# Kernel tuning notes

Measured on AMD Instinct MI355X. Metric: run time of the kernel, lower is better.

The kernel has to match this reference:

```python
import jax, jax.numpy as jnp
import numpy as np

B, T, P, H, D = 16, 32, 14, 12, 64
L = P * P           # 196 patch tokens (cls token stripped by [:, :, 1:])
DM = H * D          # 768 = d_model
S = 16              # n_synos


def _conv2d(x, w, b):
    # stride 1, padding ksize//2 with odd ksize == SAME
    y = jax.lax.conv_general_dilated(x, w, (1, 1), 'SAME',
                                     dimension_numbers=('NCHW', 'OIHW', 'NCHW'))
    return y + b[None, :, None, None]


def _layernorm(x, g, b, eps=1e-5):
    mu = x.mean(-1, keepdims=True)
    var = ((x - mu) ** 2).mean(-1, keepdims=True)
    return (x - mu) * jax.lax.rsqrt(var + eps) * g + b


def setup_inputs():
    key = jax.random.key(0)
    ks = jax.random.split(key, 8)
    return {
        'q': jax.random.normal(ks[0], (B, T, L + 1, H, D), jnp.float32),
        'k': jax.random.normal(ks[1], (B, T, L + 1, H, D), jnp.float32),
        'v': jax.random.normal(ks[2], (B, T, L + 1, H, D), jnp.float32),
        # t_conv: Conv2d(2*n_head -> 1, ksize_t=3), init normal(std=1e-3), zero bias
        't_conv_w': jax.random.normal(ks[3], (1, 2 * H, 3, 3), jnp.float32) * 1e-3,
        't_conv_b': jnp.zeros((1,), jnp.float32),
        # t_proj: LayerNorm(T^2), Linear(T^2->T), GELU, Linear(T->T^2)
        'ln_g': jnp.ones((T * T,), jnp.float32),
        'ln_b': jnp.zeros((T * T,), jnp.float32),
        'w1': jax.random.normal(ks[4], (T * T, T), jnp.float32) * 0.03,
        'b1': jnp.zeros((T,), jnp.float32),
        'w2': jax.random.normal(ks[5], (T, T * T), jnp.float32) * 0.1,
        'b2': jnp.zeros((T * T,), jnp.float32),
        # p_conv: Conv2d(T^2 -> 1, ksize_s=3)
        'p_conv_w': jax.random.normal(ks[6], (1, T * T, 3, 3), jnp.float32) * 1e-3,
        'p_conv_b': jnp.zeros((1,), jnp.float32),
        # syno_embedding (zeros in torch init; randn here for a non-degenerate test)
        'syno': jax.random.normal(ks[7], (S, DM), jnp.float32) * 0.02,
    }


def reference(q, k, v, t_conv_w, t_conv_b, ln_g, ln_b, w1, b1, w2, b2,
              p_conv_w, p_conv_b, syno):
    scale = 1.0 / jnp.sqrt(jnp.float32(D))
    # ---------------- temporal detection ----------------
    affs = []
    for a in (q, k):  # t_attrs = ['q', 'k']
        x = jnp.transpose(a[:, :, 1:], (0, 2, 1, 3, 4))      # (B, L, T, H, D)
        aff = jnp.einsum('nlqhc,nlkhc->nlqkh', x * scale, x)  # (B, L, T, T, H)
        aff = jax.nn.softmax(aff, axis=-2)                    # softmax over k
        affs.append(jnp.transpose(aff.reshape(B * L, T, T, H), (0, 3, 1, 2)))
    aff = jnp.concatenate(affs, axis=1)                       # (B*L, 2H, T, T)
    aff = _conv2d(aff, t_conv_w, t_conv_b)                    # (B*L, 1, T, T)
    aff = aff.reshape(B, P, P, T * T)                         # (B, P, P, T^2)
    h = _layernorm(aff, ln_g, ln_b)
    h = jax.nn.gelu(h @ w1 + b1, approximate=False) @ w2 + b2
    aff = aff + h
    aff = jnp.transpose(aff, (0, 3, 1, 2))                    # (B, T^2, P, P)
    y_t = _conv2d(aff, p_conv_w, p_conv_b).reshape(B, P * P)  # (B, 196)
    # ---------------- spatial detection -----------------
    kk = k[:, :, 1:].reshape(B, T, L, DM)
    vv = v[:, :, 1:].reshape(B, T, L, DM)
    s_aff = jax.nn.softmax(
        jnp.einsum('qw,ntkw->ntqk', syno / jnp.sqrt(jnp.float32(DM)), kk),
        axis=-1)                                              # (B, T, S, L)
    s_mix = jnp.einsum('ntql,ntlw->ntqw', s_aff, vv)          # (B, T, S, DM)
    y_s = s_mix.reshape(B, T * S, DM).mean(axis=1)            # (B, 768)
    return (y_t, y_s)
```

## Files before the change

kernel.cpp:

```cpp
#include <hip/hip_runtime.h>
#include <math.h>

#define T_ 32
#define P_ 14
#define H_ 12
#define D_ 64
#define L_ 196
#define DM_ 768
#define S_ 16

__global__ __launch_bounds__(256)
void temporal_kernel(const float* __restrict__ q, const float* __restrict__ k,
                     const float* __restrict__ tw, const float* __restrict__ tbias,
                     const float* __restrict__ lng, const float* __restrict__ lnb,
                     const float* __restrict__ w1, const float* __restrict__ b1,
                     const float* __restrict__ w2, const float* __restrict__ b2,
                     float* __restrict__ affbuf)
{
    const int l = blockIdx.x;
    const int b = blockIdx.y;
    const int tid = threadIdx.x;

    __shared__ float Xs[T_ * 64];
    __shared__ float As[T_ * 37];
    __shared__ float nls[1024];
    __shared__ float scratch[256];
    __shared__ float h1s[32];
    __shared__ float redv[8];

    const int pi = tid >> 3;
    const int pj = (tid & 7) << 2;
    float cacc0 = 0.f, cacc1 = 0.f, cacc2 = 0.f, cacc3 = 0.f;

    const int gi = (tid >> 4) << 1;
    const int gj = tid & 15;

    const int t_load = tid >> 3;
    const int d8 = tid & 7;

    for (int ch = 0; ch < 24; ++ch) {
        const float* src = (ch < H_) ? q : k;
        const int h = (ch < H_) ? ch : ch - H_;
        {
            const float* rowp = src + (((size_t)(b * T_ + t_load) * 197 + 1 + l) * DM_) + h * D_;
            float4 v0 = *(const float4*)(rowp + (d8 << 2));
            float4 v1 = *(const float4*)(rowp + (d8 << 2) + 32);
            const int sw = t_load & 15;
            *(float4*)&Xs[(t_load << 6) + (((d8    ) ^ sw) << 2)] = v0;
            *(float4*)&Xs[(t_load << 6) + (((d8 + 8) ^ sw) << 2)] = v1;
        }
        __syncthreads();
        {
            float g00 = 0.f, g01 = 0.f, g10 = 0.f, g11 = 0.f;
            const int swa0 = gi & 15, swa1 = (gi + 1) & 15;
            const int swb = gj;
            #pragma unroll
            for (int c4 = 0; c4 < 16; ++c4) {
                float4 a0  = *(const float4*)&Xs[( gi     << 6) + ((c4 ^ swa0) << 2)];
                float4 a1  = *(const float4*)&Xs[((gi + 1) << 6) + ((c4 ^ swa1) << 2)];
                float4 b0  = *(const float4*)&Xs[( gj     << 6) + ((c4 ^ swb) << 2)];
                float4 b1v = *(const float4*)&Xs[((gj + 16) << 6) + ((c4 ^ swb) << 2)];
                g00 += a0.x * b0.x  + a0.y * b0.y  + a0.z * b0.z  + a0.w * b0.w;
                g01 += a0.x * b1v.x + a0.y * b1v.y + a0.z * b1v.z + a0.w * b1v.w;
                g10 += a1.x * b0.x  + a1.y * b0.y  + a1.z * b0.z  + a1.w * b0.w;
                g11 += a1.x * b1v.x + a1.y * b1v.y + a1.z * b1v.z + a1.w * b1v.w;
            }
            const float scale = 0.125f;
            As[ gi      * 37 + gj     ] = g00 * scale;
            As[ gi      * 37 + gj + 16] = g01 * scale;
            As[(gi + 1) * 37 + gj     ] = g10 * scale;
            As[(gi + 1) * 37 + gj + 16] = g11 * scale;
        }
        __syncthreads();
        {
            float v0 = As[pi * 37 + pj    ];
            float v1 = As[pi * 37 + pj + 1];
            float v2 = As[pi * 37 + pj + 2];
            float v3 = As[pi * 37 + pj + 3];
            float m = fmaxf(fmaxf(v0, v1), fmaxf(v2, v3));
            m = fmaxf(m, __shfl_xor(m, 1, 8));
            m = fmaxf(m, __shfl_xor(m, 2, 8));
            m = fmaxf(m, __shfl_xor(m, 4, 8));
            v0 = __expf(v0 - m); v1 = __expf(v1 - m);
            v2 = __expf(v2 - m); v3 = __expf(v3 - m);
            float s = v0 + v1 + v2 + v3;
            s += __shfl_xor(s, 1, 8);
            s += __shfl_xor(s, 2, 8);
            s += __shfl_xor(s, 4, 8);
            float r = 1.f / s;
            As[pi * 37 + pj    ] = v0 * r;
            As[pi * 37 + pj + 1] = v1 * r;
            As[pi * 37 + pj + 2] = v2 * r;
            As[pi * 37 + pj + 3] = v3 * r;
        }
        __syncthreads();
        {
            float wc[9];
            #pragma unroll
            for (int u = 0; u < 9; ++u) wc[u] = tw[ch * 9 + u];
            #pragma unroll
            for (int di = 0; di < 3; ++di) {
                int r = pi + di - 1;
                if ((unsigned)r < (unsigned)T_) {
                    float c0 = (pj - 1 >= 0) ? As[r * 37 + pj - 1] : 0.f;
                    float c1 = As[r * 37 + pj    ];
                    float c2 = As[r * 37 + pj + 1];
                    float c3 = As[r * 37 + pj + 2];
                    float c4v = As[r * 37 + pj + 3];
                    float c5 = (pj + 4 < T_) ? As[r * 37 + pj + 4] : 0.f;
                    float w0 = wc[di * 3 + 0], wA = wc[di * 3 + 1], wB = wc[di * 3 + 2];
                    cacc0 += c0 * w0 + c1 * wA + c2 * wB;
                    cacc1 += c1 * w0 + c2 * wA + c3 * wB;
                    cacc2 += c2 * w0 + c3 * wA + c4v * wB;
                    cacc3 += c3 * w0 + c4v * wA + c5 * wB;
                }
            }
        }
        __syncthreads();
    }
    {
        float bb = tbias[0];
        cacc0 += bb; cacc1 += bb; cacc2 += bb; cacc3 += bb;
    }
    float mu, rs;
    {
        float s1 = cacc0 + cacc1 + cacc2 + cacc3;
        float s2 = cacc0 * cacc0 + cacc1 * cacc1 + cacc2 * cacc2 + cacc3 * cacc3;
        #pragma unroll
        for (int off = 32; off > 0; off >>= 1) {
            s1 += __shfl_down(s1, off);
            s2 += __shfl_down(s2, off);
        }
        if ((tid & 63) == 0) { redv[tid >> 6] = s1; redv[4 + (tid >> 6)] = s2; }
        __syncthreads();
        float t1 = redv[0] + redv[1] + redv[2] + redv[3];
        float t2 = redv[4] + redv[5] + redv[6] + redv[7];
        mu = t1 * (1.f / 1024.f);
        float var = t2 * (1.f / 1024.f) - mu * mu;
        rs = rsqrtf(var + 1e-5f);
    }
    const int tt0 = (pi << 5) + pj;
    {
        float4 g4 = *(const float4*)&lng[tt0];
        float4 b4 = *(const float4*)&lnb[tt0];
        float4 nv;
        nv.x = (cacc0 - mu) * rs * g4.x + b4.x;
        nv.y = (cacc1 - mu) * rs * g4.y + b4.y;
        nv.z = (cacc2 - mu) * rs * g4.z + b4.z;
        nv.w = (cacc3 - mu) * rs * g4.w + b4.w;
        *(float4*)&nls[tt0] = nv;
    }
    __syncthreads();
    {
        const int m = tid & 31;
        const int grp = tid >> 5;
        const int base = grp * 128;
        float p = 0.f;
        for (int u = 0; u < 128; ++u)
            p += nls[base + u] * w1[(base + u) * 32 + m];
        scratch[(m << 3) + grp] = p;
    }
    __syncthreads();
    if (tid < 32) {
        float z = b1[tid];
        #pragma unroll
        for (int g = 0; g < 8; ++g) z += scratch[(tid << 3) + g];
        z = 0.5f * z * (1.f + erff(z * 0.70710678118654752f));
        h1s[tid] = z;
    }
    __syncthreads();
    {
        float4 o4 = *(const float4*)&b2[tt0];
        #pragma unroll
        for (int m = 0; m < 32; ++m) {
            float hm = h1s[m];
            float4 w4 = *(const float4*)&w2[m * 1024 + tt0];
            o4.x += hm * w4.x; o4.y += hm * w4.y;
            o4.z += hm * w4.z; o4.w += hm * w4.w;
        }
        float4 res;
        res.x = cacc0 + o4.x; res.y = cacc1 + o4.y;
        res.z = cacc2 + o4.z; res.w = cacc3 + o4.w;
        float* outp = affbuf + (((size_t)(b * L_ + l)) << 10) + tt0;
        *(float4*)outp = res;
    }
}

__global__ __launch_bounds__(256)
void pconv_kernel(const float* __restrict__ affbuf, const float* __restrict__ pw,
                  const float* __restrict__ pb, float* __restrict__ yt)
{
    const int p = blockIdx.x;
    const int b = blockIdx.y;
    const int p1 = p / 14, p2 = p % 14;
    const int tid = threadIdx.x;
    __shared__ float pwS[9216];
    __shared__ float red4[4];
    for (int u = tid << 2; u < 9216; u += 1024)
        *(float4*)&pwS[u] = *(const float4*)&pw[u];
    __syncthreads();
    float acc = 0.f;
    #pragma unroll
    for (int di = 0; di < 3; ++di) {
        const int r = p1 + di - 1;
        if ((unsigned)r >= 14u) continue;
        #pragma unroll
        for (int dj = 0; dj < 3; ++dj) {
            const int c = p2 + dj - 1;
            if ((unsigned)c >= 14u) continue;
            const float* ap = affbuf + (((size_t)(b * 196 + r * 14 + c)) << 10);
            const int wo = di * 3 + dj;
            for (int u = tid; u < 1024; u += 256)
                acc += ap[u] * pwS[u * 9 + wo];
        }
    }
    #pragma unroll
    for (int off = 32; off > 0; off >>= 1) acc += __shfl_down(acc, off);
    if ((tid & 63) == 0) red4[tid >> 6] = acc;
    __syncthreads();
    if (tid == 0) yt[b * 196 + p] = red4[0] + red4[1] + red4[2] + red4[3] + pb[0];
}

__global__ __launch_bounds__(256)
void spatial_kernel(const float* __restrict__ k, const float* __restrict__ v,
                    const float* __restrict__ syno, float* __restrict__ ys)
{
    const int t = blockIdx.x;
    const int b = blockIdx.y;
    const int tid = threadIdx.x;
    __shared__ float Ls[16 * 208];
    __shared__ float mxs[16], sms[16];
    __shared__ float ps[196];

    const size_t base = ((size_t)(b * T_ + t) * 197 + 1) * DM_;
    const float inv_sqrt_dm = 0.036084391824352f;

    if (tid < 196) {
        const float* kp = k + base + (size_t)tid * DM_;
        float acc[16];
        #pragma unroll
        for (int s = 0; s < 16; ++s) acc[s] = 0.f;
        for (int c0 = 0; c0 < DM_; c0 += 32) {
            float4 chunk[8];
            #pragma unroll
            for (int u = 0; u < 8; ++u) chunk[u] = *(const float4*)(kp + c0 + u * 4);
            #pragma unroll
            for (int s = 0; s < 16; ++s) {
                const float* sp = syno + s * DM_ + c0;
                float a = 0.f;
                #pragma unroll
                for (int u = 0; u < 8; ++u) {
                    a += chunk[u].x * sp[u * 4 + 0] + chunk[u].y * sp[u * 4 + 1]
                       + chunk[u].z * sp[u * 4 + 2] + chunk[u].w * sp[u * 4 + 3];
                }
                acc[s] += a;
            }
        }
        #pragma unroll
        for (int s = 0; s < 16; ++s) Ls[s * 208 + tid] = acc[s] * inv_sqrt_dm;
    }
    __syncthreads();
    {
        const int s = tid >> 4, j = tid & 15;
        float m = -1e30f;
        for (int l = j; l < 196; l += 16) m = fmaxf(m, Ls[s * 208 + l]);
        #pragma unroll
        for (int msk = 1; msk < 16; msk <<= 1) m = fmaxf(m, __shfl_xor(m, msk, 16));
        float sum = 0.f;
        for (int l = j; l < 196; l += 16) sum += __expf(Ls[s * 208 + l] - m);
        #pragma unroll
        for (int msk = 1; msk < 16; msk <<= 1) sum += __shfl_xor(sum, msk, 16);
        if (j == 0) { mxs[s] = m; sms[s] = 1.f / sum; }
    }
    __syncthreads();
    if (tid < 196) {
        float p = 0.f;
        #pragma unroll
        for (int s = 0; s < 16; ++s) p += __expf(Ls[s * 208 + tid] - mxs[s]) * sms[s];
        ps[tid] = p;
    }
    __syncthreads();
    if (tid < 192) {
        const float* vp = v + base + tid * 4;
        float4 acc = {0.f, 0.f, 0.f, 0.f};
        for (int l = 0; l < 196; ++l) {
            float p = ps[l];
            float4 vv = *(const float4*)(vp + (size_t)l * DM_);
            acc.x += p * vv.x; acc.y += p * vv.y;
            acc.z += p * vv.z; acc.w += p * vv.w;
        }
        const float f = 1.f / 512.f;
        float* o = ys + b * DM_ + tid * 4;
        atomicAdd(o + 0, acc.x * f);
        atomicAdd(o + 1, acc.y * f);
        atomicAdd(o + 2, acc.z * f);
        atomicAdd(o + 3, acc.w * f);
    }
}

extern "C" void kernel_launch(void* const* d_in, const int* in_sizes, int n_in,
                              void* d_out, int out_size, void* d_ws, size_t ws_size,
                              hipStream_t stream) {
    const float* q    = (const float*)d_in[0];
    const float* k    = (const float*)d_in[1];
    const float* v    = (const float*)d_in[2];
    const float* tw   = (const float*)d_in[3];
    const float* tb   = (const float*)d_in[4];
    const float* lng  = (const float*)d_in[5];
    const float* lnb  = (const float*)d_in[6];
    const float* w1   = (const float*)d_in[7];
    const float* b1   = (const float*)d_in[8];
    const float* w2   = (const float*)d_in[9];
    const float* b2   = (const float*)d_in[10];
    const float* pw   = (const float*)d_in[11];
    const float* pb   = (const float*)d_in[12];
    const float* syno = (const float*)d_in[13];

    float* out = (float*)d_out;
    float* affbuf = (float*)d_ws;

    hipMemsetAsync(d_out, 0, (size_t)out_size * sizeof(float), stream);

    temporal_kernel<<<dim3(L_, 16), 256, 0, stream>>>(q, k, tw, tb, lng, lnb,
                                                      w1, b1, w2, b2, affbuf);
    pconv_kernel<<<dim3(L_, 16), 256, 0, stream>>>(affbuf, pw, pb, out);
    spatial_kernel<<<dim3(T_, 16), 256, 0, stream>>>(k, v, syno, out + 3136);
}
```

Before: 1.174 ms.

## Compute temporal Gram matrices with split-bf16 MFMA, one wave per channel group

Replaces the scalar FP32 dot-product Gram computation in the temporal kernel with bf16 MFMA instructions. Each input is split into hi and lo bf16 parts, and three products (hh, hl, lh) are summed to keep accuracy close to FP32. Each of the four waves now handles 6 of the 24 channels on its own, using only wave-level barriers, with register prefetch of the next channel's data, and the per-wave conv partials are summed at the end. This removes block-wide syncs and scalar FMA cost, at the price of more registers and a small precision change from the 3-term bf16 split.

```diff
diff --git a/kernel.cpp b/kernel.cpp
--- a/kernel.cpp
+++ b/kernel.cpp
@@ -8,6 +8,16 @@
 #define L_ 196
 #define DM_ 768
 #define S_ 16
+
+typedef __attribute__((ext_vector_type(8))) short short8;
+typedef __attribute__((ext_vector_type(8))) unsigned short ushort8;
+typedef __attribute__((ext_vector_type(4))) float f32x4;
+
+__device__ __forceinline__ short8 ldfrag(const char* plane, int ib, int ks, int lane) {
+    const int row = (ib << 4) + (lane & 15);
+    const int c16 = (lane >> 4) + (ks << 2);
+    return *(const short8*)(plane + row * 128 + ((c16 ^ (row & 7)) << 4));
+}
 
 __global__ __launch_bounds__(256)
 void temporal_kernel(const float* __restrict__ q, const float* __restrict__ k,
@@ -20,107 +30,177 @@
     const int l = blockIdx.x;
     const int b = blockIdx.y;
     const int tid = threadIdx.x;
-
-    __shared__ float Xs[T_ * 64];
-    __shared__ float As[T_ * 37];
-    __shared__ float nls[1024];
+    const int lane = tid & 63;
+    const int w = tid >> 6;
+
+    __shared__ __align__(16) char sm_[32768 + 18432];
     __shared__ float scratch[256];
     __shared__ float h1s[32];
     __shared__ float redv[8];
 
-    const int pi = tid >> 3;
-    const int pj = (tid & 7) << 2;
-    float cacc0 = 0.f, cacc1 = 0.f, cacc2 = 0.f, cacc3 = 0.f;
-
-    const int gi = (tid >> 4) << 1;
-    const int gj = tid & 15;
-
-    const int t_load = tid >> 3;
-    const int d8 = tid & 7;
-
-    for (int ch = 0; ch < 24; ++ch) {
+    char* XHw = sm_ + w * 8192;
+    char* XLw = XHw + 4096;
+    float* As = (float*)(sm_ + 32768 + w * 4608);
+
+    const int r = lane >> 1;
+    const int half_ = lane & 1;
+    const int hf4 = half_ << 2;
+    const int c0 = half_ << 4;
+
+    float cc16[16];
+    #pragma unroll
+    for (int i = 0; i < 16; ++i) cc16[i] = 0.f;
+
+    float4 fr[8];
+    {
+        const int ch = w * 6;
         const float* src = (ch < H_) ? q : k;
         const int h = (ch < H_) ? ch : ch - H_;
+        const float* rowp = src + (((size_t)(b * T_ + r) * 197 + 1 + l) * DM_) + h * D_ + (half_ << 5);
+        #pragma unroll
+        for (int u = 0; u < 8; ++u) fr[u] = *(const float4*)(rowp + (u << 2));
+    }
+
+    #pragma unroll
+    for (int cc = 0; cc < 6; ++cc) {
+        const int ch = w * 6 + cc;
+        ushort8 hv[4], lv[4];
+        #pragma unroll
+        for (int u4 = 0; u4 < 4; ++u4) {
+            float xs[8] = {fr[2*u4].x, fr[2*u4].y, fr[2*u4].z, fr[2*u4].w,
+                           fr[2*u4+1].x, fr[2*u4+1].y, fr[2*u4+1].z, fr[2*u4+1].w};
+            #pragma unroll
+            for (int j = 0; j < 8; ++j) {
+                const unsigned u = __float_as_uint(xs[j]);
+                const unsigned hb = (u + 0x7fffu + ((u >> 16) & 1u)) & 0xffff0000u;
+                const float res = xs[j] - __uint_as_float(hb);
+                const unsigned u2 = __float_as_uint(res);
+                const unsigned lb = u2 + 0x7fffu + ((u2 >> 16) & 1u);
+                hv[u4][j] = (unsigned short)(hb >> 16);
+                lv[u4][j] = (unsigned short)(lb >> 16);
+            }
+        }
+        if (cc < 5) {
+            const int ch2 = ch + 1;
+            const float* src = (ch2 < H_) ? q : k;
+            const int h = (ch2 < H_) ? ch2 : ch2 - H_;
+            const float* rowp = src + (((size_t)(b * T_ + r) * 197 + 1 + l) * DM_) + h * D_ + (half_ << 5);
+            #pragma unroll
+            for (int u = 0; u < 8; ++u) fr[u] = *(const float4*)(rowp + (u << 2));
+        }
+        #pragma unroll
+        for (int u4 = 0; u4 < 4; ++u4) {
+            const int sw = (((hf4 + u4) ^ (r & 7)) << 4);
+            *(ushort8*)(XHw + r * 128 + sw) = hv[u4];
+            *(ushort8*)(XLw + r * 128 + sw) = lv[u4];
+        }
+        __builtin_amdgcn_wave_barrier();
+        f32x4 a00 = {0.f, 0.f, 0.f, 0.f};
+        f32x4 a01 = a00, a10 = a00, a11 = a00;
+        #pragma unroll
+        for (int ks = 0; ks < 2; ++ks) {
+            short8 h0 = ldfrag(XHw, 0, ks, lane);
+            short8 h1 = ldfrag(XHw, 1, ks, lane);
+            short8 g0 = ldfrag(XLw, 0, ks, lane);
+            short8 g1 = ldfrag(XLw, 1, ks, lane);
+            a00 = __builtin_amdgcn_mfma_f32_16x16x32_bf16(h0, h0, a00, 0, 0, 0);
+            a01 = __builtin_amdgcn_mfma_f32_16x16x32_bf16(h0, h1, a01, 0, 0, 0);
+            a10 = __builtin_amdgcn_mfma_f32_16x16x32_bf16(h1, h0, a10, 0, 0, 0);
+            a11 = __builtin_amdgcn_mfma_f32_16x16x32_bf16(h1, h1, a11, 0, 0, 0);
+            a00 = __builtin_amdgcn_mfma_f32_16x16x32_bf16(h0, g0, a00, 0, 0, 0);
+            a01 = __builtin_amdgcn_mfma_f32_16x16x32_bf16(h0, g1, a01, 0, 0, 0);
+            a10 = __builtin_amdgcn_mfma_f32_16x16x32_bf16(h1, g0, a10, 0, 0, 0);
+            a11 = __builtin_amdgcn_mfma_f32_16x16x32_bf16(h1, g1, a11, 0, 0, 0);
+            a00 = __builtin_amdgcn_mfma_f32_16x16x32_bf16(g0, h0, a00, 0, 0, 0);
+            a01 = __builtin_amdgcn_mfma_f32_16x16x32_bf16(g0, h1, a01, 0, 0, 0);
+            a10 = __builtin_amdgcn_mfma_f32_16x16x32_bf16(g1, h0, a10, 0, 0, 0);
+            a11 = __builtin_amdgcn_mfma_f32_16x16x32_bf16(g1, h1, a11, 0, 0, 0);
+        }
         {
-            const float* rowp = src + (((size_t)(b * T_ + t_load) * 197 + 1 + l) * DM_) + h * D_;
-            float4 v0 = *(const float4*)(rowp + (d8 << 2));
-            float4 v1 = *(const float4*)(rowp + (d8 << 2) + 32);
-            const int sw = t_load & 15;
-            *(float4*)&Xs[(t_load << 6) + (((d8    ) ^ sw) << 2)] = v0;
-            *(float4*)&Xs[(t_load << 6) + (((d8 + 8) ^ sw) << 2)] = v1;
-        }
-        __syncthreads();
-        {
-            float g00 = 0.f, g01 = 0.f, g10 = 0.f, g11 = 0.f;
-            const int swa0 = gi & 15, swa1 = (gi + 1) & 15;
-            const int swb = gj;
-            #pragma unroll
-            for (int c4 = 0; c4 < 16; ++c4) {
-                float4 a0  = *(const float4*)&Xs[( gi     << 6) + ((c4 ^ swa0) << 2)];
-                float4 a1  = *(const float4*)&Xs[((gi + 1) << 6) + ((c4 ^ swa1) << 2)];
-                float4 b0  = *(const float4*)&Xs[( gj     << 6) + ((c4 ^ swb) << 2)];
-                float4 b1v = *(const float4*)&Xs[((gj + 16) << 6) + ((c4 ^ swb) << 2)];
-                g00 += a0.x * b0.x  + a0.y * b0.y  + a0.z * b0.z  + a0.w * b0.w;
-                g01 += a0.x * b1v.x + a0.y * b1v.y + a0.z * b1v.z + a0.w * b1v.w;
-                g10 += a1.x * b0.x  + a1.y * b0.y  + a1.z * b0.z  + a1.w * b0.w;
-                g11 += a1.x * b1v.x + a1.y * b1v.y + a1.z * b1v.z + a1.w * b1v.w;
-            }
-            const float scale = 0.125f;
-            As[ gi      * 37 + gj     ] = g00 * scale;
-            As[ gi      * 37 + gj + 16] = g01 * scale;
-            As[(gi + 1) * 37 + gj     ] = g10 * scale;
-            As[(gi + 1) * 37 + gj + 16] = g11 * scale;
-        }
-        __syncthreads();
-        {
-            float v0 = As[pi * 37 + pj    ];
-            float v1 = As[pi * 37 + pj + 1];
-            float v2 = As[pi * 37 + pj + 2];
-            float v3 = As[pi * 37 + pj + 3];
-            float m = fmaxf(fmaxf(v0, v1), fmaxf(v2, v3));
-            m = fmaxf(m, __shfl_xor(m, 1, 8));
-            m = fmaxf(m, __shfl_xor(m, 2, 8));
-            m = fmaxf(m, __shfl_xor(m, 4, 8));
-            v0 = __expf(v0 - m); v1 = __expf(v1 - m);
-            v2 = __expf(v2 - m); v3 = __expf(v3 - m);
-            float s = v0 + v1 + v2 + v3;
-            s += __shfl_xor(s, 1, 8);
-            s += __shfl_xor(s, 2, 8);
-            s += __shfl_xor(s, 4, 8);
-            float r = 1.f / s;
-            As[pi * 37 + pj    ] = v0 * r;
-            As[pi * 37 + pj + 1] = v1 * r;
-            As[pi * 37 + pj + 2] = v2 * r;
-            As[pi * 37 + pj + 3] = v3 * r;
-        }
-        __syncthreads();
-        {
-            float wc[9];
-            #pragma unroll
-            for (int u = 0; u < 9; ++u) wc[u] = tw[ch * 9 + u];
-            #pragma unroll
-            for (int di = 0; di < 3; ++di) {
-                int r = pi + di - 1;
-                if ((unsigned)r < (unsigned)T_) {
-                    float c0 = (pj - 1 >= 0) ? As[r * 37 + pj - 1] : 0.f;
-                    float c1 = As[r * 37 + pj    ];
-                    float c2 = As[r * 37 + pj + 1];
-                    float c3 = As[r * 37 + pj + 2];
-                    float c4v = As[r * 37 + pj + 3];
-                    float c5 = (pj + 4 < T_) ? As[r * 37 + pj + 4] : 0.f;
-                    float w0 = wc[di * 3 + 0], wA = wc[di * 3 + 1], wB = wc[di * 3 + 2];
-                    cacc0 += c0 * w0 + c1 * wA + c2 * wB;
-                    cacc1 += c1 * w0 + c2 * wA + c3 * wB;
-                    cacc2 += c2 * w0 + c3 * wA + c4v * wB;
-                    cacc3 += c3 * w0 + c4v * wA + c5 * wB;
+            const int col = lane & 15;
+            const int rbase = (lane >> 4) << 2;
+            #pragma unroll
+            for (int ib = 0; ib < 2; ++ib) {
+                #pragma unroll
+                for (int rg = 0; rg < 4; ++rg) {
+                    float gA = (ib ? a10[rg] : a00[rg]) * 0.125f;
+                    float gB = (ib ? a11[rg] : a01[rg]) * 0.125f;
+                    float m = fmaxf(gA, gB);
+                    m = fmaxf(m, __shfl_xor(m, 1, 16));
+                    m = fmaxf(m, __shfl_xor(m, 2, 16));
+                    m = fmaxf(m, __shfl_xor(m, 4, 16));
+                    m = fmaxf(m, __shfl_xor(m, 8, 16));
+                    float e0 = __expf(gA - m), e1 = __expf(gB - m);
+                    float s = e0 + e1;
+                    s += __shfl_xor(s, 1, 16);
+                    s += __shfl_xor(s, 2, 16);
+                    s += __shfl_xor(s, 4, 16);
+                    s += __shfl_xor(s, 8, 16);
+                    const float rinv = 1.f / s;
+                    const int row = (ib << 4) + rbase + rg;
+                    As[row * 36 + col] = e0 * rinv;
+                    As[row * 36 + col + 16] = e1 * rinv;
                 }
             }
         }
-        __syncthreads();
-    }
-    {
-        float bb = tbias[0];
-        cacc0 += bb; cacc1 += bb; cacc2 += bb; cacc3 += bb;
+        __builtin_amdgcn_wave_barrier();
+        {
+            float wcv[9];
+            #pragma unroll
+            for (int u = 0; u < 9; ++u) wcv[u] = tw[ch * 9 + u];
+            #pragma unroll
+            for (int dr = 0; dr < 3; ++dr) {
+                const int rr = r + dr - 1;
+                if ((unsigned)rr < 32u) {
+                    const float* rp = As + rr * 36;
+                    float vb[18];
+                    vb[0] = half_ ? rp[15] : 0.f;
+                    float4 m0 = *(const float4*)&rp[c0];
+                    float4 m1 = *(const float4*)&rp[c0 + 4];
+                    float4 m2 = *(const float4*)&rp[c0 + 8];
+                    float4 m3 = *(const float4*)&rp[c0 + 12];
+                    vb[1] = m0.x;  vb[2] = m0.y;  vb[3] = m0.z;  vb[4] = m0.w;
+                    vb[5] = m1.x;  vb[6] = m1.y;  vb[7] = m1.z;  vb[8] = m1.w;
+                    vb[9] = m2.x;  vb[10] = m2.y; vb[11] = m2.z; vb[12] = m2.w;
+                    vb[13] = m3.x; vb[14] = m3.y; vb[15] = m3.z; vb[16] = m3.w;
+                    vb[17] = half_ ? 0.f : rp[16];
+                    const float w0v = wcv[dr * 3], w1v = wcv[dr * 3 + 1], w2v = wcv[dr * 3 + 2];
+                    #pragma unroll
+                    for (int c = 0; c < 16; ++c)
+                        cc16[c] += w0v * vb[c] + w1v * vb[c + 1] + w2v * vb[c + 2];
+                }
+            }
+        }
+        __builtin_amdgcn_wave_barrier();
+    }
+    {
+        float* cpw = As;
+        #pragma unroll
+        for (int u = 0; u < 4; ++u) {
+            float4 o;
+            o.x = cc16[4 * u]; o.y = cc16[4 * u + 1];
+            o.z = cc16[4 * u + 2]; o.w = cc16[4 * u + 3];
+            *(float4*)&cpw[(r << 5) + c0 + (u << 2)] = o;
+        }
+    }
+    __syncthreads();
+
+    const int tt0 = tid << 2;
+    float cacc0, cacc1, cacc2, cacc3;
+    {
+        const float* pl0 = (const float*)(sm_ + 32768);
+        const float* pl1 = (const float*)(sm_ + 32768 + 4608);
+        const float* pl2 = (const float*)(sm_ + 32768 + 9216);
+        const float* pl3 = (const float*)(sm_ + 32768 + 13824);
+        float4 q0 = *(const float4*)&pl0[tt0];
+        float4 q1 = *(const float4*)&pl1[tt0];
+        float4 q2 = *(const float4*)&pl2[tt0];
+        float4 q3 = *(const float4*)&pl3[tt0];
+        const float bb = tbias[0];
+        cacc0 = q0.x + q1.x + q2.x + q3.x + bb;
+        cacc1 = q0.y + q1.y + q2.y + q3.y + bb;
+        cacc2 = q0.z + q1.z + q2.z + q3.z + bb;
+        cacc3 = q0.w + q1.w + q2.w + q3.w + bb;
     }
     float mu, rs;
     {
@@ -139,7 +219,7 @@
         float var = t2 * (1.f / 1024.f) - mu * mu;
         rs = rsqrtf(var + 1e-5f);
     }
-    const int tt0 = (pi << 5) + pj;
+    float* nls = (float*)sm_;
     {
         float4 g4 = *(const float4*)&lng[tt0];
         float4 b4 = *(const float4*)&lnb[tt0];
```

Result: faster. 1.113 ms (-5.2%).
